# Optimization experiments

Measured on AMD Instinct MI355X. Metric: run time of the kernel, lower is better.

The kernel has to match this reference:

```python
import jax, jax.numpy as jnp
import numpy as np

N_EMBD = 2048
N_HEAD = 16
N_KV_HEAD = 4
HEAD_DIM = N_EMBD // N_HEAD
MAX_SEQ_LEN = 2048
EPS = 1e-6
ROPE_THETA = 10000.0


def _build_rope_cache(dim, max_seq_len, theta=ROPE_THETA):
    inv_freq = 1.0 / theta ** (np.arange(0, dim, 2, dtype=np.float32) / dim)
    t = np.arange(max_seq_len, dtype=np.float32)
    freqs = np.outer(t, inv_freq)
    emb = np.concatenate([freqs, freqs], axis=-1)
    return jnp.asarray(np.cos(emb)), jnp.asarray(np.sin(emb))


def _rotate_half(x):
    x1, x2 = jnp.split(x, 2, axis=-1)
    return jnp.concatenate([-x2, x1], axis=-1)


def _rms_norm(x, w, eps=EPS):
    var = jnp.mean(jnp.square(x), axis=-1, keepdims=True)
    return x * jax.lax.rsqrt(var + eps) * w


def setup_inputs() -> dict:
    key = jax.random.key(0)
    ks = jax.random.split(key, 7)
    s = 1.0 / np.sqrt(N_EMBD)
    kv_dim = N_KV_HEAD * HEAD_DIM
    x = jax.random.normal(ks[0], (2, 2048, N_EMBD), dtype=jnp.float32)
    Wq = jax.random.normal(ks[1], (N_EMBD, N_EMBD), dtype=jnp.float32) * s
    Wk = jax.random.normal(ks[2], (kv_dim, N_EMBD), dtype=jnp.float32) * s
    Wv = jax.random.normal(ks[3], (kv_dim, N_EMBD), dtype=jnp.float32) * s
    Wo = jax.random.normal(ks[4], (N_EMBD, N_EMBD), dtype=jnp.float32) * s
    qn_w = jnp.ones((HEAD_DIM,), dtype=jnp.float32)
    kn_w = jnp.ones((HEAD_DIM,), dtype=jnp.float32)
    cos, sin = _build_rope_cache(HEAD_DIM, MAX_SEQ_LEN)
    return {"x": x, "Wq": Wq, "Wk": Wk, "Wv": Wv, "Wo": Wo,
            "qn_w": qn_w, "kn_w": kn_w, "rope_cos": cos, "rope_sin": sin}


def reference(x, Wq, Wk, Wv, Wo, qn_w, kn_w, rope_cos, rope_sin):
    B, T, C = x.shape
    # projections (torch Linear: y = x @ W.T)
    q = jnp.einsum('btc,dc->btd', x, Wq).reshape(B, T, N_HEAD, HEAD_DIM).transpose(0, 2, 1, 3)
    k = jnp.einsum('btc,dc->btd', x, Wk).reshape(B, T, N_KV_HEAD, HEAD_DIM).transpose(0, 2, 1, 3)
    v = jnp.einsum('btc,dc->btd', x, Wv).reshape(B, T, N_KV_HEAD, HEAD_DIM).transpose(0, 2, 1, 3)
    # qk rms-norm
    q = _rms_norm(q, qn_w)
    k = _rms_norm(k, kn_w)
    # rope
    cos = rope_cos[:T][None, None]  # [1,1,T,D]
    sin = rope_sin[:T][None, None]
    q = q * cos + _rotate_half(q) * sin
    k = k * cos + _rotate_half(k) * sin
    # GQA broadcast: group queries over kv heads instead of repeating k/v
    G = N_HEAD // N_KV_HEAD
    qg = q.reshape(B, N_KV_HEAD, G, T, HEAD_DIM)
    scale = 1.0 / jnp.sqrt(jnp.asarray(HEAD_DIM, dtype=q.dtype))
    scores = jnp.einsum('bhgqd,bhkd->bhgqk', qg, k) * scale  # [B,KV,G,T,T]
    causal = jnp.tril(jnp.ones((T, T), dtype=bool))
    scores = jnp.where(causal, scores, jnp.asarray(-jnp.inf, dtype=scores.dtype))
    attn = jax.nn.softmax(scores, axis=-1)
    y = jnp.einsum('bhgqk,bhkd->bhgqd', attn, v)  # [B,KV,G,T,D]
    y = y.reshape(B, N_HEAD, T, HEAD_DIM).transpose(0, 2, 1, 3).reshape(B, T, C)
    return jnp.einsum('btc,dc->btd', y, Wo)
```

## Files before the change

### kernel.cpp

```cpp
#include <hip/hip_runtime.h>
#include <stdint.h>

typedef unsigned short u16;
typedef __attribute__((ext_vector_type(4))) float f32x4;
typedef __attribute__((ext_vector_type(16))) float f32x16;
typedef __attribute__((ext_vector_type(8))) short bf16x8;
typedef __attribute__((ext_vector_type(4))) unsigned short u16x4;
typedef __attribute__((ext_vector_type(4))) unsigned u32x4;

static __device__ __forceinline__ u16 f2bf(float f) {
  union { float f; unsigned u; } v; v.f = f;
  unsigned r = v.u + 0x7fffu + ((v.u >> 16) & 1u);
  return (u16)(r >> 16);
}

static __device__ __forceinline__ unsigned cvtpk(float lo, float hi) {
  unsigned r;
  asm("v_cvt_pk_bf16_f32 %0, %1, %2" : "=v"(r) : "v"(lo), "v"(hi));
  return r;
}

static __device__ __forceinline__ void plane32_swap(unsigned& a, unsigned& b) {
  asm volatile("v_permlane32_swap_b32 %0, %1" : "+v"(a), "+v"(b));
}

static __device__ __forceinline__ void load_lds16(const void* g, void* l) {
  __builtin_amdgcn_global_load_lds(
      (const __attribute__((address_space(1))) void*)g,
      (__attribute__((address_space(3))) void*)l, 16, 0, 0);
}


__global__ __launch_bounds__(256) void cvt_f32_bf16(
    const float* __restrict__ in, u16* __restrict__ out, int n) {
  int i = blockIdx.x * 256 + threadIdx.x;
  const int n4 = n >> 2;
  for (; i < n4; i += gridDim.x * 256) {
    f32x4 v = *(const f32x4*)(in + (size_t)i * 4);
    u16x4 o = { f2bf(v[0]), f2bf(v[1]), f2bf(v[2]), f2bf(v[3]) };
    *(u16x4*)(out + (size_t)i * 4) = o;
  }
}

__global__ __launch_bounds__(256) void build_wcat(
    const float* __restrict__ Wq, const float* __restrict__ Wk,
    const float* __restrict__ Wv, u16* __restrict__ out) {
  int i = blockIdx.x * 256 + threadIdx.x;
  const int n4 = 3072 * 512;
  for (; i < n4; i += gridDim.x * 256) {
    int row = i >> 9;
    int c4 = i & 511;
    const float* src;
    if (row < 2048)       src = Wq + (size_t)row * 2048;
    else if (row < 2560)  src = Wk + (size_t)(row - 2048) * 2048;
    else                  src = Wv + (size_t)(row - 2560) * 2048;
    f32x4 v = *(const f32x4*)(src + c4 * 4);
    u16x4 o = { f2bf(v[0]), f2bf(v[1]), f2bf(v[2]), f2bf(v[3]) };
    *(u16x4*)(out + (size_t)i * 4) = o;
  }
}

__global__ __launch_bounds__(256) void gemm_bt(
    const u16* __restrict__ A, const u16* __restrict__ B,
    float* __restrict__ C, int M, int N, int K) {
  __shared__ u16 As[128 * 32];
  __shared__ u16 Bs[128 * 32];
  const int tid = threadIdx.x;
  const int lin = blockIdx.x;
  const int x = lin & 7, t = lin >> 3;
  const int bm = x * 4 + (t & 3);
  const int bn = t >> 2;
  const int w = tid >> 6, l = tid & 63;
  const int wr = w >> 1, wc = w & 1;
  const int lr = l & 15, lg = l >> 4;
  f32x4 acc[4][4] = {};
  const int srow = tid >> 2;
  const int scol = (tid & 3) << 3;
  const u16* Ag = A + (size_t)bm * 128 * K + (size_t)srow * K + scol;
  const u16* Bg = B + (size_t)bn * 128 * K + (size_t)srow * K + scol;
  u16* Asl = As + srow * 32 + scol;
  u16* Bsl = Bs + srow * 32 + scol;
  const int nk = K >> 5;
  for (int kt = 0; kt < nk; ++kt) {
    __syncthreads();
    const int ko = kt << 5;
    load_lds16(Ag + ko, Asl);
    load_lds16(Ag + (size_t)64 * K + ko, Asl + 64 * 32);
    load_lds16(Bg + ko, Bsl);
    load_lds16(Bg + (size_t)64 * K + ko, Bsl + 64 * 32);
    __syncthreads();
    bf16x8 af[4], bfr[4];
#pragma unroll
    for (int m = 0; m < 4; ++m)
      af[m] = *(const bf16x8*)&As[(wr * 64 + m * 16 + lr) * 32 + lg * 8];
#pragma unroll
    for (int n = 0; n < 4; ++n)
      bfr[n] = *(const bf16x8*)&Bs[(wc * 64 + n * 16 + lr) * 32 + lg * 8];
#pragma unroll
    for (int m = 0; m < 4; ++m)
#pragma unroll
      for (int n = 0; n < 4; ++n)
        acc[m][n] = __builtin_amdgcn_mfma_f32_16x16x32_bf16(af[m], bfr[n], acc[m][n], 0, 0, 0);
  }
#pragma unroll
  for (int m = 0; m < 4; ++m) {
    const int row = bm * 128 + wr * 64 + m * 16 + lg * 4;
#pragma unroll
    for (int n = 0; n < 4; ++n) {
      const int col = bn * 128 + wc * 64 + n * 16 + lr;
#pragma unroll
      for (int r = 0; r < 4; ++r)
        C[(size_t)(row + r) * N + col] = acc[m][n][r];
    }
  }
}

__global__ __launch_bounds__(256) void norm_rope(
    const float* __restrict__ qkv, const float* __restrict__ qn_w,
    const float* __restrict__ kn_w, const float* __restrict__ cosb,
    const float* __restrict__ sinb, u16* __restrict__ qhat,
    u16* __restrict__ khat) {
  const int gw = (blockIdx.x * 256 + threadIdx.x) >> 6;
  const int lane = threadIdx.x & 63;
  const int slot = gw % 20;
  const int row = gw / 20;
  const int t = row & 2047;
  const int b = row >> 11;
  const float* src; const float* nw; u16* dst;
  bool isq = slot < 16;
  if (isq) {
    src = qkv + (size_t)row * 3072 + slot * 128;
    nw = qn_w;
    dst = qhat + ((size_t)(b * 16 + slot) * 2048 + t) * 128;
  } else {
    src = qkv + (size_t)row * 3072 + 2048 + (slot - 16) * 128;
    nw = kn_w;
    dst = khat + ((size_t)(b * 4 + (slot - 16)) * 2048 + t) * 128;
  }
  float x1 = src[lane], x2 = src[lane + 64];
  float ss = x1 * x1 + x2 * x2;
#pragma unroll
  for (int o = 32; o; o >>= 1) ss += __shfl_xor(ss, o);
  float rs = rsqrtf(ss * (1.0f / 128.0f) + 1e-6f);
  float h1 = x1 * rs * nw[lane];
  float h2 = x2 * rs * nw[lane + 64];
  float c = cosb[t * 128 + lane], s = sinb[t * 128 + lane];
  float o1 = h1 * c - h2 * s;
  float o2 = h2 * c + h1 * s;
  if (isq) { o1 *= 0.088388347648318447f; o2 *= 0.088388347648318447f; }
  dst[lane] = f2bf(o1);
  dst[lane + 64] = f2bf(o2);
}

__global__ __launch_bounds__(256) void v_trans(
    const float* __restrict__ qkv, u16* __restrict__ vT) {
  __shared__ u16 st[64][130];
  const int bi = blockIdx.x;
  const int tt = bi & 31;
  const int kv = (bi >> 5) & 3;
  const int b = bi >> 7;
  const int tid = threadIdx.x;
#pragma unroll
  for (int i = 0; i < 32; ++i) {
    int idx = i * 256 + tid;
    int t = idx >> 7, d = idx & 127;
    float v = qkv[(size_t)(b * 2048 + tt * 64 + t) * 3072 + 2560 + kv * 128 + d];
    st[t][d] = f2bf(v);
  }
  __syncthreads();
#pragma unroll
  for (int i = 0; i < 32; ++i) {
    int idx = i * 256 + tid;
    int d = idx >> 6, t = idx & 63;
    vT[((size_t)(b * 4 + kv) * 128 + d) * 2048 + tt * 64 + t] = st[t][d];
  }
}

__global__ __launch_bounds__(512, 2) void attn(
    const u16* __restrict__ qhat, const u16* __restrict__ khat,
    const u16* __restrict__ vT, u16* __restrict__ yb) {
  __shared__ u16 Kt[2][64 * 128];
  const int bi = blockIdx.x;
  const int s = bi & 7;
  const int bh = bi >> 3;
  const int h = bh & 15, b = bh >> 4;
  const int kvh = h >> 2;
  const int tid = threadIdx.x;
  const int w = tid >> 6, l = tid & 63;
  const int ws = w & 3;
  const int cw = (w < 4) ? s : (15 - s);
  const int ql = l & 31, hi = l >> 5;
  const int wq0 = cw * 128 + ws * 32;
  const int wq_end = wq0 + 31;
  const int qg = wq0 + ql;

  bf16x8 qf[8];
  const u16* qp = qhat + ((size_t)(b * 16 + h) * 2048 + qg) * 128 + hi * 8;
#pragma unroll
  for (int sf = 0; sf < 8; ++sf) qf[sf] = *(const bf16x8*)(qp + 16 * sf);

  f32x16 yacc[4] = {};
  float m = -1e30f, lsum = 0.f;

  const u16* Kg = khat + (size_t)(b * 4 + kvh) * 2048 * 128;
  const u16* Vg = vT + (size_t)(b * 4 + kvh) * 128 * 2048;
  const int nt = 32 - 2 * s;

  auto stageK = [&](int tile, int buf) {
#pragma unroll
    for (int j = 0; j < 2; ++j) {
      int idx = j * 512 + tid;
      int row = idx >> 4, ch = idx & 15;
      load_lds16(Kg + (size_t)(tile * 64 + row) * 128 + ((ch ^ (row & 7)) * 8),
                 &Kt[buf][idx * 8]);
    }
  };

  stageK(0, 0);
  int cur = 0;
  for (int tile = 0; tile < nt; ++tile) {
    const int kv0 = tile * 64;
    __syncthreads();
    if (tile + 1 < nt) stageK(tile + 1, cur ^ 1);
    if (kv0 <= wq_end) {
      const u16* Vrow = Vg + (size_t)ql * 2048 + kv0 + hi * 8;
      bf16x8 va[4], vb[4];
#pragma unroll
      for (int ks = 0; ks < 4; ++ks) va[ks] = *(const bf16x8*)(Vrow + ks * 16);
#pragma unroll
      for (int ks = 0; ks < 4; ++ks) vb[ks] = *(const bf16x8*)(Vrow + 32 * 2048 + ks * 16);
      const u16* Kc = Kt[cur];
      f32x16 sacc[2] = {};
      __builtin_amdgcn_s_setprio(1);
#pragma unroll
      for (int n = 0; n < 2; ++n) {
#pragma unroll
        for (int sf = 0; sf < 8; ++sf) {
          bf16x8 kf = *(const bf16x8*)&Kc[(n * 32 + ql) * 128 + (((2 * sf + hi) ^ (l & 7)) * 8)];
          sacc[n] = __builtin_amdgcn_mfma_f32_32x32x16_bf16(kf, qf[sf], sacc[n], 0, 0, 0);
        }
      }
      __builtin_amdgcn_s_setprio(0);
      if (kv0 + 63 > wq0) {
#pragma unroll
        for (int n = 0; n < 2; ++n)
#pragma unroll
          for (int r = 0; r < 16; ++r) {
            int kv = kv0 + n * 32 + (r & 3) + 8 * (r >> 2) + 4 * hi;
            if (kv > qg) sacc[n][r] = -1e30f;
          }
      }
      float pm = -1e30f;
#pragma unroll
      for (int n = 0; n < 2; ++n)
#pragma unroll
        for (int r = 0; r < 16; ++r) pm = fmaxf(pm, sacc[n][r]);
      pm = fmaxf(pm, __shfl_xor(pm, 32));
      if (!__all(pm - m <= 8.0f)) {
        float mn = fmaxf(m, pm);
        float sc = __expf(m - mn);
        m = mn;
        lsum *= sc;
#pragma unroll
        for (int r = 0; r < 16; ++r) {
          int row = (r & 3) + 8 * (r >> 2) + 4 * hi;
          float scr = __shfl(sc, row);
#pragma unroll
          for (int d = 0; d < 4; ++d) yacc[d][r] *= scr;
        }
      }
      float ls = 0.f;
#pragma unroll
      for (int n = 0; n < 2; ++n)
#pragma unroll
        for (int r = 0; r < 16; ++r) {
          float e = __expf(sacc[n][r] - m);
          sacc[n][r] = e;
          ls += e;
        }
      ls += __shfl_xor(ls, 32);
      lsum += ls;
      bf16x8 pa[4];
#pragma unroll
      for (int s4 = 0; s4 < 4; ++s4) {
        const int n = s4 >> 1, R = (s4 & 1) * 8;
        unsigned P01 = cvtpk(sacc[n][R + 0], sacc[n][R + 1]);
        unsigned P23 = cvtpk(sacc[n][R + 2], sacc[n][R + 3]);
        unsigned P45 = cvtpk(sacc[n][R + 4], sacc[n][R + 5]);
        unsigned P67 = cvtpk(sacc[n][R + 6], sacc[n][R + 7]);
        plane32_swap(P01, P45);
        plane32_swap(P23, P67);
        union { u32x4 u; bf16x8 bv; } cvu;
        cvu.u[0] = P01; cvu.u[1] = P23; cvu.u[2] = P45; cvu.u[3] = P67;
        pa[s4] = cvu.bv;
      }
      __builtin_amdgcn_s_setprio(1);
#pragma unroll
      for (int ks = 0; ks < 4; ++ks)
        yacc[0] = __builtin_amdgcn_mfma_f32_32x32x16_bf16(pa[ks], va[ks], yacc[0], 0, 0, 0);
#pragma unroll
      for (int ks = 0; ks < 4; ++ks) va[ks] = *(const bf16x8*)(Vrow + 64 * 2048 + ks * 16);
#pragma unroll
      for (int ks = 0; ks < 4; ++ks)
        yacc[1] = __builtin_amdgcn_mfma_f32_32x32x16_bf16(pa[ks], vb[ks], yacc[1], 0, 0, 0);
#pragma unroll
      for (int ks = 0; ks < 4; ++ks) vb[ks] = *(const bf16x8*)(Vrow + 96 * 2048 + ks * 16);
#pragma unroll
      for (int ks = 0; ks < 4; ++ks)
        yacc[2] = __builtin_amdgcn_mfma_f32_32x32x16_bf16(pa[ks], va[ks], yacc[2], 0, 0, 0);
#pragma unroll
      for (int ks = 0; ks < 4; ++ks)
        yacc[3] = __builtin_amdgcn_mfma_f32_32x32x16_bf16(pa[ks], vb[ks], yacc[3], 0, 0, 0);
      __builtin_amdgcn_s_setprio(0);
    }
    cur ^= 1;
  }
#pragma unroll
  for (int r = 0; r < 16; ++r) {
    int row = (r & 3) + 8 * (r >> 2) + 4 * hi;
    float li = __shfl(lsum, row);
    float inv = 1.0f / li;
    u16* yp = yb + ((size_t)(b * 2048) + wq0 + row) * 2048 + h * 128 + ql;
#pragma unroll
    for (int d = 0; d < 4; ++d) yp[d * 32] = f2bf(yacc[d][r] * inv);
  }
}


extern "C" void kernel_launch(void* const* d_in, const int* in_sizes, int n_in,
                              void* d_out, int out_size, void* d_ws, size_t ws_size,
                              hipStream_t stream) {
  const float* x    = (const float*)d_in[0];
  const float* Wq   = (const float*)d_in[1];
  const float* Wk   = (const float*)d_in[2];
  const float* Wv   = (const float*)d_in[3];
  const float* Wo   = (const float*)d_in[4];
  const float* qn   = (const float*)d_in[5];
  const float* kn   = (const float*)d_in[6];
  const float* cosb = (const float*)d_in[7];
  const float* sinb = (const float*)d_in[8];
  float* out = (float*)d_out;
  (void)in_sizes; (void)n_in; (void)out_size; (void)ws_size;

  char* p = (char*)d_ws;
  u16*   xb   = (u16*)p;   p += (size_t)8388608 * 2;
  u16*   wcat = (u16*)p;   p += (size_t)6291456 * 2;
  u16*   wob  = (u16*)p;   p += (size_t)4194304 * 2;
  float* qkvf = (float*)p; p += (size_t)12582912 * 4;
  u16*   qh   = (u16*)p;   p += (size_t)8388608 * 2;
  u16*   kh   = (u16*)p;   p += (size_t)2097152 * 2;
  u16*   vt   = (u16*)p;   p += (size_t)2097152 * 2;
  u16*   yb   = (u16*)p;   p += (size_t)8388608 * 2;

  cvt_f32_bf16<<<2048, 256, 0, stream>>>(x, xb, 8388608);
  build_wcat<<<2048, 256, 0, stream>>>(Wq, Wk, Wv, wcat);
  cvt_f32_bf16<<<2048, 256, 0, stream>>>(Wo, wob, 4194304);
  gemm_bt<<<768, 256, 0, stream>>>(xb, wcat, qkvf, 4096, 3072, 2048);
  norm_rope<<<20480, 256, 0, stream>>>(qkvf, qn, kn, cosb, sinb, qh, kh);
  v_trans<<<256, 256, 0, stream>>>(qkvf, vt);
  attn<<<256, 512, 0, stream>>>(qh, kh, vt, yb);
  gemm_bt<<<512, 256, 0, stream>>>(yb, wob, out, 4096, 2048, 2048);
}
```

Before: 261.1 us.

## Stage V tiles through LDS and use exp2 with log2e-folded scale

V tiles are now double-buffered into LDS with async global-to-LDS loads and a swizzled layout, alongside K. The PV MFMAs read V fragments from LDS instead of issuing direct global loads from each wave, so the V traffic is shared across the 8 waves of the block. The softmax switches to the native v_exp_f32 (base-2), with log2(e) folded into the Q scale and the rescale threshold adjusted to match. In exchange, LDS usage per block doubles, which may limit occupancy at two blocks per CU.

```diff
diff --git a/kernel.cpp b/kernel.cpp
--- a/kernel.cpp
+++ b/kernel.cpp
@@ -22,6 +22,12 @@
 
 static __device__ __forceinline__ void plane32_swap(unsigned& a, unsigned& b) {
   asm volatile("v_permlane32_swap_b32 %0, %1" : "+v"(a), "+v"(b));
+}
+
+static __device__ __forceinline__ float exp2_fast(float x) {
+  float r;
+  asm("v_exp_f32 %0, %1" : "=v"(r) : "v"(x));
+  return r;
 }
 
 static __device__ __forceinline__ void load_lds16(const void* g, void* l) {
@@ -147,7 +153,7 @@
   float c = cosb[t * 128 + lane], s = sinb[t * 128 + lane];
   float o1 = h1 * c - h2 * s;
   float o2 = h2 * c + h1 * s;
-  if (isq) { o1 *= 0.088388347648318447f; o2 *= 0.088388347648318447f; }
+  if (isq) { o1 *= 0.12751744752f; o2 *= 0.12751744752f; }
   dst[lane] = f2bf(o1);
   dst[lane + 64] = f2bf(o2);
 }
@@ -180,6 +186,7 @@
     const u16* __restrict__ qhat, const u16* __restrict__ khat,
     const u16* __restrict__ vT, u16* __restrict__ yb) {
   __shared__ u16 Kt[2][64 * 128];
+  __shared__ u16 Vt[2][128 * 64];
   const int bi = blockIdx.x;
   const int s = bi & 7;
   const int bh = bi >> 3;
@@ -215,21 +222,26 @@
                  &Kt[buf][idx * 8]);
     }
   };
+  auto stageV = [&](int tile, int buf) {
+#pragma unroll
+    for (int j = 0; j < 2; ++j) {
+      int idx = j * 512 + tid;
+      int row = idx >> 3, ch = idx & 7;
+      load_lds16(Vg + (size_t)row * 2048 + tile * 64 + ((ch ^ (row & 7)) * 8),
+                 &Vt[buf][idx * 8]);
+    }
+  };
 
   stageK(0, 0);
+  stageV(0, 0);
   int cur = 0;
   for (int tile = 0; tile < nt; ++tile) {
     const int kv0 = tile * 64;
     __syncthreads();
-    if (tile + 1 < nt) stageK(tile + 1, cur ^ 1);
+    if (tile + 1 < nt) { stageK(tile + 1, cur ^ 1); stageV(tile + 1, cur ^ 1); }
     if (kv0 <= wq_end) {
-      const u16* Vrow = Vg + (size_t)ql * 2048 + kv0 + hi * 8;
-      bf16x8 va[4], vb[4];
-#pragma unroll
-      for (int ks = 0; ks < 4; ++ks) va[ks] = *(const bf16x8*)(Vrow + ks * 16);
-#pragma unroll
-      for (int ks = 0; ks < 4; ++ks) vb[ks] = *(const bf16x8*)(Vrow + 32 * 2048 + ks * 16);
       const u16* Kc = Kt[cur];
+      const u16* Vc = Vt[cur];
       f32x16 sacc[2] = {};
       __builtin_amdgcn_s_setprio(1);
 #pragma unroll
@@ -256,9 +268,9 @@
 #pragma unroll
         for (int r = 0; r < 16; ++r) pm = fmaxf(pm, sacc[n][r]);
       pm = fmaxf(pm, __shfl_xor(pm, 32));
-      if (!__all(pm - m <= 8.0f)) {
+      if (!__all(pm - m <= 11.0f)) {
         float mn = fmaxf(m, pm);
-        float sc = __expf(m - mn);
+        float sc = exp2_fast(m - mn);
         m = mn;
         lsum *= sc;
 #pragma unroll
@@ -274,7 +286,7 @@
       for (int n = 0; n < 2; ++n)
 #pragma unroll
         for (int r = 0; r < 16; ++r) {
-          float e = __expf(sacc[n][r] - m);
+          float e = exp2_fast(sacc[n][r] - m);
           sacc[n][r] = e;
           ls += e;
         }
@@ -296,21 +308,14 @@
       }
       __builtin_amdgcn_s_setprio(1);
 #pragma unroll
-      for (int ks = 0; ks < 4; ++ks)
-        yacc[0] = __builtin_amdgcn_mfma_f32_32x32x16_bf16(pa[ks], va[ks], yacc[0], 0, 0, 0);
-#pragma unroll
-      for (int ks = 0; ks < 4; ++ks) va[ks] = *(const bf16x8*)(Vrow + 64 * 2048 + ks * 16);
-#pragma unroll
-      for (int ks = 0; ks < 4; ++ks)
-        yacc[1] = __builtin_amdgcn_mfma_f32_32x32x16_bf16(pa[ks], vb[ks], yacc[1], 0, 0, 0);
-#pragma unroll
-      for (int ks = 0; ks < 4; ++ks) vb[ks] = *(const bf16x8*)(Vrow + 96 * 2048 + ks * 16);
-#pragma unroll
-      for (int ks = 0; ks < 4; ++ks)
-        yacc[2] = __builtin_amdgcn_mfma_f32_32x32x16_bf16(pa[ks], va[ks], yacc[2], 0, 0, 0);
-#pragma unroll
-      for (int ks = 0; ks < 4; ++ks)
-        yacc[3] = __builtin_amdgcn_mfma_f32_32x32x16_bf16(pa[ks], vb[ks], yacc[3], 0, 0, 0);
+      for (int d = 0; d < 4; ++d) {
+        const int rv = d * 32 + ql;
+#pragma unroll
+        for (int ks = 0; ks < 4; ++ks) {
+          bf16x8 vf = *(const bf16x8*)&Vc[rv * 64 + (((ks * 2 + hi) ^ (rv & 7)) * 8)];
+          yacc[d] = __builtin_amdgcn_mfma_f32_32x32x16_bf16(pa[ks], vf, yacc[d], 0, 0, 0);
+        }
+      }
       __builtin_amdgcn_s_setprio(0);
     }
     cur ^= 1;
```

Result: faster. 242.1 us (-7.3%).
